# Kernel tuning notes

Measured on AMD Instinct MI355X. Metric: run time of the kernel, lower is better.

Reference implementation:

```python
import jax, jax.numpy as jnp
import numpy as np

H = 1024      # hidden_dim
V = 50257     # output_dim (vocab)
L = 512       # max_length


def setup_inputs() -> dict:
    key = jax.random.key(0)
    ks = jax.random.split(key, 12)
    s = 0.02
    return {
        "x": jax.random.randint(ks[0], (1,), 0, V),
        "hidden": jax.random.normal(ks[1], (1, 1, H), jnp.float32),
        "encoder_outputs": jax.random.normal(ks[2], (L, H), jnp.float32),
        "emb": jax.random.normal(ks[3], (V, H), jnp.float32) * s,
        "Ww": jax.random.normal(ks[4], (L, 2 * H), jnp.float32) * s,
        "bw": jnp.zeros((L,), jnp.float32),
        "Wc": jax.random.normal(ks[5], (H, 2 * H), jnp.float32) * s,
        "bc": jnp.zeros((H,), jnp.float32),
        "Wih": jax.random.normal(ks[6], (3 * H, H), jnp.float32) * s,
        "Whh": jax.random.normal(ks[7], (3 * H, H), jnp.float32) * s,
        "bih": jnp.zeros((3 * H,), jnp.float32),
        "bhh": jnp.zeros((3 * H,), jnp.float32),
        "Wo": jax.random.normal(ks[8], (V, H), jnp.float32) * s,
        "bo": jnp.zeros((V,), jnp.float32),
    }


def reference(x, hidden, encoder_outputs, emb, Ww, bw, Wc, bc, Wih, Whh, bih, bhh, Wo, bo):
    embed = emb[x].reshape(1, 1, -1)                      # [1,1,H]
    cat1 = jnp.concatenate([embed[0], hidden[0]], axis=1)  # [1,2H]
    weights = jax.nn.softmax(cat1 @ Ww.T + bw, axis=1)     # [1,L]
    wctx = weights @ encoder_outputs                       # [1,H]
    out = jnp.concatenate([embed[0], wctx], axis=1) @ Wc.T + bc  # [1,H]
    out = jax.nn.relu(out)
    # GRU cell (PyTorch gate layout: r, z, n)
    gi = out @ Wih.T + bih                                 # [1,3H]
    gh = hidden[0] @ Whh.T + bhh                           # [1,3H]
    r = jax.nn.sigmoid(gi[:, :H] + gh[:, :H])
    z = jax.nn.sigmoid(gi[:, H:2 * H] + gh[:, H:2 * H])
    n = jnp.tanh(gi[:, 2 * H:] + r * gh[:, 2 * H:])
    h_new = (1.0 - z) * n + z * hidden[0]                  # [1,H]
    logits = h_new @ Wo.T + bo                             # [1,V]
    out = jax.nn.log_softmax(logits, axis=1)
    return out, h_new[None], weights
```

## Files before the change

### kernel.cpp

```cpp
#include <hip/hip_runtime.h>
#include <math.h>

#define Hdim 1024
#define Vdim 50257
#define Ldim 512

__device__ __forceinline__ float waveReduceSum(float v) {
    #pragma unroll
    for (int off = 32; off > 0; off >>= 1) v += __shfl_down(v, off, 64);
    return v;
}
__device__ __forceinline__ float waveReduceMax(float v) {
    #pragma unroll
    for (int off = 32; off > 0; off >>= 1) v = fmaxf(v, __shfl_down(v, off, 64));
    return v;
}
template<int NW>
__device__ __forceinline__ float blockReduceSum(float v, float* red) {
    v = waveReduceSum(v);
    const int lane = threadIdx.x & 63, wid = threadIdx.x >> 6;
    if (lane == 0) red[wid] = v;
    __syncthreads();
    float s = red[0];
    #pragma unroll
    for (int i = 1; i < NW; i++) s += red[i];
    __syncthreads();
    return s;
}

__global__ __launch_bounds__(256) void k_att_gh(
    const int* __restrict__ xp, const float* __restrict__ hidden,
    const float* __restrict__ emb, const float* __restrict__ Ww,
    const float* __restrict__ bw, const float* __restrict__ Whh,
    const float* __restrict__ bhh, float* __restrict__ att, float* __restrict__ gh)
{
    __shared__ float red[4];
    const int t = threadIdx.x, bid = blockIdx.x;
    float acc = 0.f;
    if (bid < Ldim) {
        const int tok = xp[0];
        const float4* wrow = (const float4*)(Ww + (size_t)bid * (2 * Hdim));
        const float4* ev   = (const float4*)(emb + (size_t)tok * Hdim);
        const float4* hv   = (const float4*)hidden;
        #pragma unroll
        for (int k = 0; k < 2; ++k) {
            const int j = t * 2 + k;
            const float4 w = wrow[j];
            const float4 c = (j < Hdim / 4) ? ev[j] : hv[j - Hdim / 4];
            acc += w.x * c.x + w.y * c.y + w.z * c.z + w.w * c.w;
        }
        acc = blockReduceSum<4>(acc, red);
        if (t == 0) att[bid] = acc + bw[bid];
    } else {
        const int r = bid - Ldim;
        const float4* wrow = (const float4*)(Whh + (size_t)r * Hdim);
        const float4 w = wrow[t];
        const float4 h = ((const float4*)hidden)[t];
        acc = w.x * h.x + w.y * h.y + w.z * h.z + w.w * h.w;
        acc = blockReduceSum<4>(acc, red);
        if (t == 0) gh[r] = acc + bhh[r];
    }
}

__global__ __launch_bounds__(512) void k_softmax(
    const float* __restrict__ att, float* __restrict__ weights,
    float* __restrict__ out_w, float* __restrict__ wctx)
{
    __shared__ float red[8];
    __shared__ float bm, bs;
    const int t = threadIdx.x;
    const float v = att[t];
    float m = waveReduceMax(v);
    if ((t & 63) == 0) red[t >> 6] = m;
    __syncthreads();
    if (t == 0) {
        float mm = red[0];
        #pragma unroll
        for (int i = 1; i < 8; i++) mm = fmaxf(mm, red[i]);
        bm = mm;
    }
    __syncthreads();
    const float e = __expf(v - bm);
    float s = waveReduceSum(e);
    __syncthreads();
    if ((t & 63) == 0) red[t >> 6] = s;
    __syncthreads();
    if (t == 0) {
        float ss = red[0];
        #pragma unroll
        for (int i = 1; i < 8; i++) ss += red[i];
        bs = ss;
    }
    __syncthreads();
    const float w = e / bs;
    weights[t] = w;
    out_w[t]   = w;
    wctx[t] = 0.f; wctx[t + 512] = 0.f;
}

__global__ __launch_bounds__(256) void k_wctx(
    const float* __restrict__ weights, const float* __restrict__ enc,
    float* __restrict__ wctx)
{
    const int b = blockIdx.x, t = threadIdx.x;
    float4 acc = make_float4(0.f, 0.f, 0.f, 0.f);
    #pragma unroll
    for (int i = 0; i < 8; ++i) {
        const int l = b * 8 + i;
        const float w = weights[l];
        const float4 e = ((const float4*)(enc + (size_t)l * Hdim))[t];
        acc.x += w * e.x; acc.y += w * e.y; acc.z += w * e.z; acc.w += w * e.w;
    }
    atomicAdd(&wctx[t * 4 + 0], acc.x);
    atomicAdd(&wctx[t * 4 + 1], acc.y);
    atomicAdd(&wctx[t * 4 + 2], acc.z);
    atomicAdd(&wctx[t * 4 + 3], acc.w);
}

__global__ __launch_bounds__(256) void k_wc(
    const int* __restrict__ xp, const float* __restrict__ emb,
    const float* __restrict__ wctx, const float* __restrict__ Wc,
    const float* __restrict__ bc, float* __restrict__ cvec)
{
    __shared__ float red[4];
    const int t = threadIdx.x, r = blockIdx.x;
    const int tok = xp[0];
    const float4* wrow = (const float4*)(Wc + (size_t)r * (2 * Hdim));
    const float4* ev   = (const float4*)(emb + (size_t)tok * Hdim);
    const float4* cv   = (const float4*)wctx;
    float acc = 0.f;
    #pragma unroll
    for (int k = 0; k < 2; ++k) {
        const int j = t * 2 + k;
        const float4 w = wrow[j];
        const float4 c = (j < Hdim / 4) ? ev[j] : cv[j - Hdim / 4];
        acc += w.x * c.x + w.y * c.y + w.z * c.z + w.w * c.w;
    }
    acc = blockReduceSum<4>(acc, red);
    if (t == 0) cvec[r] = fmaxf(acc + bc[r], 0.f);
}

__global__ __launch_bounds__(256) void k_gru(
    const float* __restrict__ Wih, const float* __restrict__ bih,
    const float* __restrict__ gh, const float* __restrict__ cvec,
    const float* __restrict__ hidden, float* __restrict__ hnew,
    float* __restrict__ out_h)
{
    __shared__ float red[4];
    const int t = threadIdx.x, j = blockIdx.x;
    const float4 c = ((const float4*)cvec)[t];
    const float4 a = ((const float4*)(Wih + (size_t)j * Hdim))[t];
    const float4 b = ((const float4*)(Wih + (size_t)(j + Hdim) * Hdim))[t];
    const float4 d = ((const float4*)(Wih + (size_t)(j + 2 * Hdim) * Hdim))[t];
    float s0 = a.x * c.x + a.y * c.y + a.z * c.z + a.w * c.w;
    float s1 = b.x * c.x + b.y * c.y + b.z * c.z + b.w * c.w;
    float s2 = d.x * c.x + d.y * c.y + d.z * c.z + d.w * c.w;
    s0 = blockReduceSum<4>(s0, red);
    s1 = blockReduceSum<4>(s1, red);
    s2 = blockReduceSum<4>(s2, red);
    if (t == 0) {
        const float gir = s0 + bih[j];
        const float giz = s1 + bih[j + Hdim];
        const float gin = s2 + bih[j + 2 * Hdim];
        const float rr = 1.f / (1.f + __expf(-(gir + gh[j])));
        const float zz = 1.f / (1.f + __expf(-(giz + gh[j + Hdim])));
        const float nn = tanhf(gin + rr * gh[j + 2 * Hdim]);
        const float h = (1.f - zz) * nn + zz * hidden[j];
        hnew[j]  = h;
        out_h[j] = h;
    }
}

__global__ __launch_bounds__(256) void k_logits(
    const float* __restrict__ Wo, const float* __restrict__ bo,
    const float* __restrict__ h, float* __restrict__ logits)
{
    __shared__ float red[4];
    const int r = blockIdx.x, t = threadIdx.x;
    const float4 w = ((const float4*)(Wo + (size_t)r * Hdim))[t];
    const float4 hv = ((const float4*)h)[t];
    float acc = w.x * hv.x + w.y * hv.y + w.z * hv.z + w.w * hv.w;
    acc = waveReduceSum(acc);
    if ((t & 63) == 0) red[t >> 6] = acc;
    __syncthreads();
    if (t == 0) logits[r] = red[0] + red[1] + red[2] + red[3] + bo[r];
}

__global__ __launch_bounds__(256) void k_lse_part(
    const float* __restrict__ logits, float* __restrict__ pm, float* __restrict__ ps)
{
    __shared__ float redm[4], reds[4];
    const int gid = blockIdx.x * 256 + threadIdx.x;
    float m = -1e30f, s = 0.f;
    for (int i = gid; i < Vdim; i += 64 * 256) {
        const float v = logits[i];
        const float nm = fmaxf(m, v);
        s = s * __expf(m - nm) + __expf(v - nm);
        m = nm;
    }
    #pragma unroll
    for (int off = 32; off > 0; off >>= 1) {
        const float om = __shfl_down(m, off, 64);
        const float os = __shfl_down(s, off, 64);
        const float nm = fmaxf(m, om);
        s = s * __expf(m - nm) + os * __expf(om - nm);
        m = nm;
    }
    const int lane = threadIdx.x & 63, wid = threadIdx.x >> 6;
    if (lane == 0) { redm[wid] = m; reds[wid] = s; }
    __syncthreads();
    if (threadIdx.x == 0) {
        float M = redm[0], S = reds[0];
        #pragma unroll
        for (int i = 1; i < 4; i++) {
            const float nm = fmaxf(M, redm[i]);
            S = S * __expf(M - nm) + reds[i] * __expf(redm[i] - nm);
            M = nm;
        }
        pm[blockIdx.x] = M; ps[blockIdx.x] = S;
    }
}

__global__ __launch_bounds__(64) void k_lse_final(
    const float* __restrict__ pm, const float* __restrict__ ps,
    float* __restrict__ logZ)
{
    const int t = threadIdx.x;
    float m = pm[t], s = ps[t];
    #pragma unroll
    for (int off = 32; off > 0; off >>= 1) {
        const float om = __shfl_down(m, off, 64);
        const float os = __shfl_down(s, off, 64);
        const float nm = fmaxf(m, om);
        s = s * __expf(m - nm) + os * __expf(om - nm);
        m = nm;
    }
    if (t == 0) logZ[0] = m + logf(s);
}

__global__ __launch_bounds__(256) void k_out(
    float* __restrict__ out, const float* __restrict__ logZ)
{
    const int i = blockIdx.x * 256 + threadIdx.x;
    if (i < Vdim) out[i] = out[i] - logZ[0];
}

extern "C" void kernel_launch(void* const* d_in, const int* in_sizes, int n_in,
                              void* d_out, int out_size, void* d_ws, size_t ws_size,
                              hipStream_t stream)
{
    const int*   x      = (const int*)  d_in[0];
    const float* hidden = (const float*)d_in[1];
    const float* enc    = (const float*)d_in[2];
    const float* emb    = (const float*)d_in[3];
    const float* Ww     = (const float*)d_in[4];
    const float* bw     = (const float*)d_in[5];
    const float* Wc     = (const float*)d_in[6];
    const float* bc     = (const float*)d_in[7];
    const float* Wih    = (const float*)d_in[8];
    const float* Whh    = (const float*)d_in[9];
    const float* bih    = (const float*)d_in[10];
    const float* bhh    = (const float*)d_in[11];
    const float* Wo     = (const float*)d_in[12];
    const float* bo     = (const float*)d_in[13];

    float* out      = (float*)d_out;
    float* out_logp = out;
    float* out_h    = out + Vdim;
    float* out_w    = out + Vdim + Hdim;

    float* ws      = (float*)d_ws;
    float* att     = ws;
    float* weights = ws + 512;
    float* wctx    = ws + 1024;
    float* cvec    = ws + 2048;
    float* gh      = ws + 3072;
    float* hnew    = ws + 6144;
    float* pm      = ws + 7168;
    float* psum    = ws + 7232;
    float* logZ    = ws + 7296;

    k_att_gh   <<<dim3(Ldim + 3 * Hdim), dim3(256), 0, stream>>>(x, hidden, emb, Ww, bw, Whh, bhh, att, gh);
    k_softmax  <<<dim3(1),               dim3(512), 0, stream>>>(att, weights, out_w, wctx);
    k_wctx     <<<dim3(64),              dim3(256), 0, stream>>>(weights, enc, wctx);
    k_wc       <<<dim3(Hdim),            dim3(256), 0, stream>>>(x, emb, wctx, Wc, bc, cvec);
    k_gru      <<<dim3(Hdim),            dim3(256), 0, stream>>>(Wih, bih, gh, cvec, hidden, hnew, out_h);
    k_logits   <<<dim3(Vdim),            dim3(256), 0, stream>>>(Wo, bo, hnew, out_logp);
    k_lse_part <<<dim3(64),              dim3(256), 0, stream>>>(out_logp, pm, psum);
    k_lse_final<<<dim3(1),               dim3(64),  0, stream>>>(pm, psum, logZ);
    k_out      <<<dim3((Vdim + 255) / 256), dim3(256), 0, stream>>>(out_logp, logZ);
}
```

Before: 415.9 us.

## Fuse softmax into wctx, logits into partial LSE, and LSE final into output

```diff
diff --git a/kernel.cpp b/kernel.cpp
--- a/kernel.cpp
+++ b/kernel.cpp
@@ -4,6 +4,8 @@
 #define Hdim 1024
 #define Vdim 50257
 #define Ldim 512
+
+#define LOGITS_BLOCKS 2048
 
 __device__ __forceinline__ float waveReduceSum(float v) {
     #pragma unroll
@@ -32,7 +34,8 @@
     const int* __restrict__ xp, const float* __restrict__ hidden,
     const float* __restrict__ emb, const float* __restrict__ Ww,
     const float* __restrict__ bw, const float* __restrict__ Whh,
-    const float* __restrict__ bhh, float* __restrict__ att, float* __restrict__ gh)
+    const float* __restrict__ bhh, float* __restrict__ att,
+    float* __restrict__ gh, float* __restrict__ wctx)
 {
     __shared__ float red[4];
     const int t = threadIdx.x, bid = blockIdx.x;
@@ -53,6 +56,7 @@
         if (t == 0) att[bid] = acc + bw[bid];
     } else {
         const int r = bid - Ldim;
+        if (r < 4) wctx[r * 256 + t] = 0.f;
         const float4* wrow = (const float4*)(Whh + (size_t)r * Hdim);
         const float4 w = wrow[t];
         const float4 h = ((const float4*)hidden)[t];
@@ -62,52 +66,39 @@
     }
 }
 
-__global__ __launch_bounds__(512) void k_softmax(
-    const float* __restrict__ att, float* __restrict__ weights,
+__global__ __launch_bounds__(256) void k_soft_wctx(
+    const float* __restrict__ att, const float* __restrict__ enc,
     float* __restrict__ out_w, float* __restrict__ wctx)
 {
-    __shared__ float red[8];
+    __shared__ float red[4];
+    __shared__ float wsm[512];
     __shared__ float bm, bs;
-    const int t = threadIdx.x;
-    const float v = att[t];
-    float m = waveReduceMax(v);
-    if ((t & 63) == 0) red[t >> 6] = m;
-    __syncthreads();
-    if (t == 0) {
-        float mm = red[0];
-        #pragma unroll
-        for (int i = 1; i < 8; i++) mm = fmaxf(mm, red[i]);
-        bm = mm;
-    }
-    __syncthreads();
-    const float e = __expf(v - bm);
-    float s = waveReduceSum(e);
-    __syncthreads();
-    if ((t & 63) == 0) red[t >> 6] = s;
-    __syncthreads();
-    if (t == 0) {
-        float ss = red[0];
-        #pragma unroll
-        for (int i = 1; i < 8; i++) ss += red[i];
-        bs = ss;
-    }
-    __syncthreads();
-    const float w = e / bs;
-    weights[t] = w;
-    out_w[t]   = w;
-    wctx[t] = 0.f; wctx[t + 512] = 0.f;
-}
-
-__global__ __launch_bounds__(256) void k_wctx(
-    const float* __restrict__ weights, const float* __restrict__ enc,
-    float* __restrict__ wctx)
-{
-    const int b = blockIdx.x, t = threadIdx.x;
+    const int t = threadIdx.x, b = blockIdx.x;
+    const int lane = t & 63, wid = t >> 6;
+
+    const float v0 = att[t], v1 = att[t + 256];
+    float m = waveReduceMax(fmaxf(v0, v1));
+    if (lane == 0) red[wid] = m;
+    __syncthreads();
+    if (t == 0) bm = fmaxf(fmaxf(red[0], red[1]), fmaxf(red[2], red[3]));
+    __syncthreads();
+    const float e0 = __expf(v0 - bm), e1 = __expf(v1 - bm);
+    float s = waveReduceSum(e0 + e1);
+    if (lane == 0) red[wid] = s;
+    __syncthreads();
+    if (t == 0) bs = red[0] + red[1] + red[2] + red[3];
+    __syncthreads();
+    const float inv = 1.f / bs;
+    const float w0 = e0 * inv, w1 = e1 * inv;
+    wsm[t] = w0; wsm[t + 256] = w1;
+    if (b == 0) { out_w[t] = w0; out_w[t + 256] = w1; }
+    __syncthreads();
+
     float4 acc = make_float4(0.f, 0.f, 0.f, 0.f);
     #pragma unroll
     for (int i = 0; i < 8; ++i) {
         const int l = b * 8 + i;
-        const float w = weights[l];
+        const float w = wsm[l];
         const float4 e = ((const float4*)(enc + (size_t)l * Hdim))[t];
         acc.x += w * e.x; acc.y += w * e.y; acc.z += w * e.z; acc.w += w * e.w;
     }
@@ -171,45 +162,36 @@
     }
 }
 
-__global__ __launch_bounds__(256) void k_logits(
+__global__ __launch_bounds__(256) void k_logits_lse(
     const float* __restrict__ Wo, const float* __restrict__ bo,
-    const float* __restrict__ h, float* __restrict__ logits)
-{
-    __shared__ float red[4];
-    const int r = blockIdx.x, t = threadIdx.x;
-    const float4 w = ((const float4*)(Wo + (size_t)r * Hdim))[t];
-    const float4 hv = ((const float4*)h)[t];
-    float acc = w.x * hv.x + w.y * hv.y + w.z * hv.z + w.w * hv.w;
-    acc = waveReduceSum(acc);
-    if ((t & 63) == 0) red[t >> 6] = acc;
-    __syncthreads();
-    if (t == 0) logits[r] = red[0] + red[1] + red[2] + red[3] + bo[r];
-}
-
-__global__ __launch_bounds__(256) void k_lse_part(
-    const float* __restrict__ logits, float* __restrict__ pm, float* __restrict__ ps)
+    const float* __restrict__ h, float* __restrict__ logits,
+    float* __restrict__ pm, float* __restrict__ ps)
 {
     __shared__ float redm[4], reds[4];
-    const int gid = blockIdx.x * 256 + threadIdx.x;
+    const int t = threadIdx.x, lane = t & 63, wid = t >> 6;
+    const float4* h4 = (const float4*)h;
+    const float4 hv0 = h4[lane], hv1 = h4[lane + 64],
+                 hv2 = h4[lane + 128], hv3 = h4[lane + 192];
     float m = -1e30f, s = 0.f;
-    for (int i = gid; i < Vdim; i += 64 * 256) {
-        const float v = logits[i];
-        const float nm = fmaxf(m, v);
-        s = s * __expf(m - nm) + __expf(v - nm);
+    for (int r = blockIdx.x * 4 + wid; r < Vdim; r += LOGITS_BLOCKS * 4) {
+        const float4* w4 = (const float4*)(Wo + (size_t)r * Hdim);
+        const float4 a0 = w4[lane], a1 = w4[lane + 64],
+                     a2 = w4[lane + 128], a3 = w4[lane + 192];
+        float acc = a0.x*hv0.x + a0.y*hv0.y + a0.z*hv0.z + a0.w*hv0.w
+                  + a1.x*hv1.x + a1.y*hv1.y + a1.z*hv1.z + a1.w*hv1.w
+                  + a2.x*hv2.x + a2.y*hv2.y + a2.z*hv2.z + a2.w*hv2.w
+                  + a3.x*hv3.x + a3.y*hv3.y + a3.z*hv3.z + a3.w*hv3.w;
+        #pragma unroll
+        for (int off = 32; off > 0; off >>= 1) acc += __shfl_xor(acc, off, 64);
+        const float lg = acc + bo[r];
+        if (lane == 0) logits[r] = lg;
+        const float nm = fmaxf(m, lg);
+        s = s * __expf(m - nm) + __expf(lg - nm);
         m = nm;
     }
-    #pragma unroll
-    for (int off = 32; off > 0; off >>= 1) {
-        const float om = __shfl_down(m, off, 64);
-        const float os = __shfl_down(s, off, 64);
-        const float nm = fmaxf(m, om);
-        s = s * __expf(m - nm) + os * __expf(om - nm);
-        m = nm;
-    }
-    const int lane = threadIdx.x & 63, wid = threadIdx.x >> 6;
     if (lane == 0) { redm[wid] = m; reds[wid] = s; }
     __syncthreads();
-    if (threadIdx.x == 0) {
+    if (t == 0) {
         float M = redm[0], S = reds[0];
         #pragma unroll
         for (int i = 1; i < 4; i++) {
@@ -221,28 +203,45 @@
     }
 }
 
-__global__ __launch_bounds__(64) void k_lse_final(
+__global__ __launch_bounds__(256) void k_lse_out(
     const float* __restrict__ pm, const float* __restrict__ ps,
-    float* __restrict__ logZ)
-{
-    const int t = threadIdx.x;
-    float m = pm[t], s = ps[t];
-    #pragma unroll
-    for (int off = 32; off > 0; off >>= 1) {
-        const float om = __shfl_down(m, off, 64);
-        const float os = __shfl_down(s, off, 64);
+    float* __restrict__ out)
+{
+    __shared__ float redm[4], reds[4];
+    __shared__ float slz;
+    const int t = threadIdx.x, lane = t & 63, wid = t >> 6;
+    float m = -1e30f, s = 0.f;
+    #pragma unroll
+    for (int i = t; i < LOGITS_BLOCKS; i += 256) {
+        const float om = pm[i], os = ps[i];
         const float nm = fmaxf(m, om);
         s = s * __expf(m - nm) + os * __expf(om - nm);
         m = nm;
     }
-    if (t == 0) logZ[0] = m + logf(s);
-}
-
-__global__ __launch_bounds__(256) void k_out(
-    float* __restrict__ out, const float* __restrict__ logZ)
-{
-    const int i = blockIdx.x * 256 + threadIdx.x;
-    if (i < Vdim) out[i] = out[i] - logZ[0];
+    #pragma unroll
+    for (int off = 32; off > 0; off >>= 1) {
+        const float om = __shfl_xor(m, off, 64);
+        const float os = __shfl_xor(s, off, 64);
+        const float nm = fmaxf(m, om);
+        s = s * __expf(m - nm) + os * __expf(om - nm);
+        m = nm;
+    }
+    if (lane == 0) { redm[wid] = m; reds[wid] = s; }
+    __syncthreads();
+    if (t == 0) {
+        float M = redm[0], S = reds[0];
+        #pragma unroll
+        for (int i = 1; i < 4; i++) {
+            const float nm = fmaxf(M, redm[i]);
+            S = S * __expf(M - nm) + reds[i] * __expf(redm[i] - nm);
+            M = nm;
+        }
+        slz = M + logf(S);
+    }
+    __syncthreads();
+    const float lz = slz;
+    for (int i = blockIdx.x * 256 + t; i < Vdim; i += gridDim.x * 256)
+        out[i] -= lz;
 }
 
 extern "C" void kernel_launch(void* const* d_in, const int* in_sizes, int n_in,
@@ -269,24 +268,19 @@
     float* out_h    = out + Vdim;
     float* out_w    = out + Vdim + Hdim;
 
-    float* ws      = (float*)d_ws;
-    float* att     = ws;
-    float* weights = ws + 512;
-    float* wctx    = ws + 1024;
-    float* cvec    = ws + 2048;
-    float* gh      = ws + 3072;
-    float* hnew    = ws + 6144;
-    float* pm      = ws + 7168;
-    float* psum    = ws + 7232;
-    float* logZ    = ws + 7296;
-
-    k_att_gh   <<<dim3(Ldim + 3 * Hdim), dim3(256), 0, stream>>>(x, hidden, emb, Ww, bw, Whh, bhh, att, gh);
-    k_softmax  <<<dim3(1),               dim3(512), 0, stream>>>(att, weights, out_w, wctx);
-    k_wctx     <<<dim3(64),              dim3(256), 0, stream>>>(weights, enc, wctx);
-    k_wc       <<<dim3(Hdim),            dim3(256), 0, stream>>>(x, emb, wctx, Wc, bc, cvec);
-    k_gru      <<<dim3(Hdim),            dim3(256), 0, stream>>>(Wih, bih, gh, cvec, hidden, hnew, out_h);
-    k_logits   <<<dim3(Vdim),            dim3(256), 0, stream>>>(Wo, bo, hnew, out_logp);
-    k_lse_part <<<dim3(64),              dim3(256), 0, stream>>>(out_logp, pm, psum);
-    k_lse_final<<<dim3(1),               dim3(64),  0, stream>>>(pm, psum, logZ);
-    k_out      <<<dim3((Vdim + 255) / 256), dim3(256), 0, stream>>>(out_logp, logZ);
-}
+    float* ws   = (float*)d_ws;
+    float* att  = ws;
+    float* wctx = ws + 512;
+    float* cvec = ws + 1536;
+    float* gh   = ws + 2560;
+    float* hnew = ws + 5632;
+    float* pm   = ws + 6656;
+    float* psum = ws + 6656 + LOGITS_BLOCKS;
+
+    k_att_gh    <<<dim3(Ldim + 3 * Hdim), dim3(256), 0, stream>>>(x, hidden, emb, Ww, bw, Whh, bhh, att, gh, wctx);
+    k_soft_wctx <<<dim3(64),              dim3(256), 0, stream>>>(att, enc, out_w, wctx);
+    k_wc        <<<dim3(Hdim),            dim3(256), 0, stream>>>(x, emb, wctx, Wc, bc, cvec);
+    k_gru       <<<dim3(Hdim),            dim3(256), 0, stream>>>(Wih, bih, gh, cvec, hidden, hnew, out_h);
+    k_logits_lse<<<dim3(LOGITS_BLOCKS),   dim3(256), 0, stream>>>(Wo, bo, hnew, out_logp, pm, psum);
+    k_lse_out   <<<dim3(64),              dim3(256), 0, stream>>>(pm, psum, out_logp);
+}
```

Result: slower. 424.6 us (+2.1%).
